# Kernel optimization log

Hardware: AMD Instinct MI355X
Metric: run time of the kernel (lower is better)

## Reference

```python
import jax, jax.numpy as jnp
import numpy as np

B, D_IN, UNITS = 16384, 4096, 4096
EPS = 1e-05

def setup_inputs() -> dict:
    key = jax.random.key(0)
    k1, k2 = jax.random.split(key)
    x = jax.random.normal(k1, (B, D_IN), dtype=jnp.float32)
    # glorot_uniform init for Dense kernel
    limit = np.sqrt(6.0 / (D_IN + UNITS)).astype(np.float32)
    W = jax.random.uniform(k2, (D_IN, UNITS), dtype=jnp.float32, minval=-limit, maxval=limit)
    b = jnp.zeros((UNITS,), dtype=jnp.float32)
    return {"x": x, "W": W, "b": b}

def reference(x, W, b):
    # L2-normalize each row (tf.norm axis=1, keepdims) with +1e-5 stabilizer
    x_norm = jnp.sqrt(jnp.sum(x * x, axis=1, keepdims=True)) + EPS  # [B,1]
    x_dir = x / x_norm                                              # [B,D]
    # dense + bias + ReLU
    return jax.nn.relu(x_dir @ W + b)                               # [B,UNITS]
```

## Files before the change

### kernel.cpp

```cpp
#include <hip/hip_runtime.h>

#define BROWS 16384
#define DIN   4096
#define NOUT  4096
#define EPSV  1e-5f

typedef __attribute__((ext_vector_type(8))) short short8;
typedef __attribute__((ext_vector_type(4))) float f32x4;

__device__ __forceinline__ unsigned short f32_to_bf16(float f) {
    union { float f; unsigned u; } v;
    v.f = f;
    unsigned r = (v.u + 0x7fffu + ((v.u >> 16) & 1u)) >> 16;
    return (unsigned short)r;
}

__global__ __launch_bounds__(256) void normalize_cast_kernel(
    const float* __restrict__ x, unsigned short* __restrict__ A) {
    const int row = blockIdx.x;
    const int tid = threadIdx.x;
    const float4* xr = (const float4*)(x + (size_t)row * DIN);
    float4 v[4];
    float ss = 0.f;
#pragma unroll
    for (int i = 0; i < 4; ++i) {
        v[i] = xr[tid + i * 256];
        ss += v[i].x * v[i].x + v[i].y * v[i].y + v[i].z * v[i].z + v[i].w * v[i].w;
    }
#pragma unroll
    for (int o = 32; o > 0; o >>= 1) ss += __shfl_down(ss, o);
    __shared__ float red[4];
    const int wave = tid >> 6, lane = tid & 63;
    if (lane == 0) red[wave] = ss;
    __syncthreads();
    const float inv = 1.f / (sqrtf(red[0] + red[1] + red[2] + red[3]) + EPSV);
    uint2* Ar = (uint2*)(A + (size_t)row * DIN);
#pragma unroll
    for (int i = 0; i < 4; ++i) {
        uint2 p;
        p.x = (unsigned)f32_to_bf16(v[i].x * inv) | ((unsigned)f32_to_bf16(v[i].y * inv) << 16);
        p.y = (unsigned)f32_to_bf16(v[i].z * inv) | ((unsigned)f32_to_bf16(v[i].w * inv) << 16);
        Ar[tid + i * 256] = p;
    }
}

__global__ __launch_bounds__(256) void transpose_cast_kernel(
    const float* __restrict__ W, unsigned short* __restrict__ Wt) {
    __shared__ float tile[32][33];
    const int bn = blockIdx.x * 32, bk = blockIdx.y * 32;
    const int t = threadIdx.x;
    const int lk = t >> 3, ln4 = (t & 7) * 4;
    float4 v = *(const float4*)(W + (size_t)(bk + lk) * NOUT + bn + ln4);
    tile[lk][ln4 + 0] = v.x;
    tile[lk][ln4 + 1] = v.y;
    tile[lk][ln4 + 2] = v.z;
    tile[lk][ln4 + 3] = v.w;
    __syncthreads();
    const int ln = t >> 3, lk4 = (t & 7) * 4;
    uint2 p;
    p.x = (unsigned)f32_to_bf16(tile[lk4 + 0][ln]) | ((unsigned)f32_to_bf16(tile[lk4 + 1][ln]) << 16);
    p.y = (unsigned)f32_to_bf16(tile[lk4 + 2][ln]) | ((unsigned)f32_to_bf16(tile[lk4 + 3][ln]) << 16);
    *(uint2*)(Wt + (size_t)(bn + ln) * DIN + bk + lk4) = p;
}


__device__ __forceinline__ void async_copy16(const unsigned short* g, unsigned short* l) {
    __builtin_amdgcn_global_load_lds(
        (const __attribute__((address_space(1))) unsigned int*)g,
        (__attribute__((address_space(3))) unsigned int*)l, 16, 0, 0);
}

__global__ __launch_bounds__(256, 2) void gemm_bias_relu_kernel(
    const unsigned short* __restrict__ A, const unsigned short* __restrict__ Wt,
    const float* __restrict__ bias, float* __restrict__ C) {
    __shared__ __align__(16) unsigned short As[128 * 32];
    __shared__ __align__(16) unsigned short Bs[128 * 32];
    const int tid = threadIdx.x;
    const int wave = tid >> 6, lane = tid & 63;
    const int m0 = blockIdx.y * 128, n0 = blockIdx.x * 128;
    const int wr = (wave >> 1) * 64, wc = (wave & 1) * 64;
    const int lm = lane & 15;
    const int lk8 = (lane >> 4) * 8;

    f32x4 acc[4][4] = {};

    const int c0 = tid, c1 = tid + 256;
    const unsigned short* gA0 = A + (size_t)(m0 + (c0 >> 2)) * DIN + (c0 & 3) * 8;
    const unsigned short* gA1 = A + (size_t)(m0 + (c1 >> 2)) * DIN + (c1 & 3) * 8;
    const unsigned short* gB0 = Wt + (size_t)(n0 + (c0 >> 2)) * DIN + (c0 & 3) * 8;
    const unsigned short* gB1 = Wt + (size_t)(n0 + (c1 >> 2)) * DIN + (c1 & 3) * 8;
    unsigned short* lA0 = &As[(c0 & ~63) * 8];
    unsigned short* lA1 = &As[(c1 & ~63) * 8];
    unsigned short* lB0 = &Bs[(c0 & ~63) * 8];
    unsigned short* lB1 = &Bs[(c1 & ~63) * 8];

    for (int k0 = 0; k0 < DIN; k0 += 32) {
        __syncthreads();
        async_copy16(gA0 + k0, lA0);
        async_copy16(gA1 + k0, lA1);
        async_copy16(gB0 + k0, lB0);
        async_copy16(gB1 + k0, lB1);
        __syncthreads();

        short8 af[4], bf[4];
#pragma unroll
        for (int i = 0; i < 4; ++i)
            af[i] = *(const short8*)(&As[(wr + i * 16 + lm) * 32 + lk8]);
#pragma unroll
        for (int j = 0; j < 4; ++j)
            bf[j] = *(const short8*)(&Bs[(wc + j * 16 + lm) * 32 + lk8]);
#pragma unroll
        for (int i = 0; i < 4; ++i)
#pragma unroll
            for (int j = 0; j < 4; ++j)
                acc[i][j] = __builtin_amdgcn_mfma_f32_16x16x32_bf16(af[i], bf[j], acc[i][j], 0, 0, 0);
    }

    float bj[4];
#pragma unroll
    for (int j = 0; j < 4; ++j) bj[j] = bias[n0 + wc + j * 16 + lm];
    const int colb = n0 + wc + lm;
    const int rowb = m0 + wr + ((lane >> 4) << 2);
#pragma unroll
    for (int i = 0; i < 4; ++i) {
#pragma unroll
        for (int r = 0; r < 4; ++r) {
            float* cp = C + (size_t)(rowb + i * 16 + r) * NOUT + colb;
#pragma unroll
            for (int j = 0; j < 4; ++j) {
                float v = acc[i][j][r] + bj[j];
                cp[j * 16] = v > 0.f ? v : 0.f;
            }
        }
    }
}

extern "C" void kernel_launch(void* const* d_in, const int* in_sizes, int n_in,
                              void* d_out, int out_size, void* d_ws, size_t ws_size,
                              hipStream_t stream) {
    const float* x = (const float*)d_in[0];
    const float* W = (const float*)d_in[1];
    const float* b = (const float*)d_in[2];
    float* out = (float*)d_out;

    unsigned short* Abf = (unsigned short*)d_ws;
    unsigned short* Wt = Abf + (size_t)BROWS * DIN;

    normalize_cast_kernel<<<BROWS, 256, 0, stream>>>(x, Abf);
    transpose_cast_kernel<<<dim3(NOUT / 32, DIN / 32), 256, 0, stream>>>(W, Wt);
    gemm_bias_relu_kernel<<<dim3(NOUT / 128, BROWS / 128), 256, 0, stream>>>(Abf, Wt, b, out);
}
```

Before: 1.082 ms.

## Swizzle GEMM LDS layout, use nontemporal output stores, enlarge transpose tiles

The GEMM now XOR-swizzles the k-chunk position in LDS per row, both when filling it through global_load_lds and when reading MFMA fragments, to reduce LDS bank conflicts on the short8 reads. Output stores become nontemporal so the large fp32 result bypasses cache retention. The W transpose/cast kernel moves to 64x64 tiles with four loads per thread to amortise launch and sync overhead. The swizzle must stay consistent between the global source offsets and the fragment reads, or results will be wrong.

After: 1.070 ms. Within noise of the previous version (-1.1%).

```diff
diff --git a/kernel.cpp b/kernel.cpp
--- a/kernel.cpp
+++ b/kernel.cpp
@@ -46,21 +46,28 @@
 
 __global__ __launch_bounds__(256) void transpose_cast_kernel(
     const float* __restrict__ W, unsigned short* __restrict__ Wt) {
-    __shared__ float tile[32][33];
-    const int bn = blockIdx.x * 32, bk = blockIdx.y * 32;
+    __shared__ float tile[64][65];
+    const int bn = blockIdx.x * 64, bk = blockIdx.y * 64;
     const int t = threadIdx.x;
-    const int lk = t >> 3, ln4 = (t & 7) * 4;
-    float4 v = *(const float4*)(W + (size_t)(bk + lk) * NOUT + bn + ln4);
-    tile[lk][ln4 + 0] = v.x;
-    tile[lk][ln4 + 1] = v.y;
-    tile[lk][ln4 + 2] = v.z;
-    tile[lk][ln4 + 3] = v.w;
+    const int lk = t >> 4, ln4 = (t & 15) * 4;
+#pragma unroll
+    for (int i = 0; i < 4; ++i) {
+        float4 v = *(const float4*)(W + (size_t)(bk + lk + i * 16) * NOUT + bn + ln4);
+        tile[lk + i * 16][ln4 + 0] = v.x;
+        tile[lk + i * 16][ln4 + 1] = v.y;
+        tile[lk + i * 16][ln4 + 2] = v.z;
+        tile[lk + i * 16][ln4 + 3] = v.w;
+    }
     __syncthreads();
-    const int ln = t >> 3, lk4 = (t & 7) * 4;
-    uint2 p;
-    p.x = (unsigned)f32_to_bf16(tile[lk4 + 0][ln]) | ((unsigned)f32_to_bf16(tile[lk4 + 1][ln]) << 16);
-    p.y = (unsigned)f32_to_bf16(tile[lk4 + 2][ln]) | ((unsigned)f32_to_bf16(tile[lk4 + 3][ln]) << 16);
-    *(uint2*)(Wt + (size_t)(bn + ln) * DIN + bk + lk4) = p;
+    const int ln = t >> 4, lk4 = (t & 15) * 4;
+#pragma unroll
+    for (int i = 0; i < 4; ++i) {
+        const int n = ln + i * 16;
+        uint2 p;
+        p.x = (unsigned)f32_to_bf16(tile[lk4 + 0][n]) | ((unsigned)f32_to_bf16(tile[lk4 + 1][n]) << 16);
+        p.y = (unsigned)f32_to_bf16(tile[lk4 + 2][n]) | ((unsigned)f32_to_bf16(tile[lk4 + 3][n]) << 16);
+        *(uint2*)(Wt + (size_t)(bn + n) * DIN + bk + lk4) = p;
+    }
 }
 
 
@@ -80,15 +87,19 @@
     const int m0 = blockIdx.y * 128, n0 = blockIdx.x * 128;
     const int wr = (wave >> 1) * 64, wc = (wave & 1) * 64;
     const int lm = lane & 15;
-    const int lk8 = (lane >> 4) * 8;
+    const int q = lane >> 4;
+    const int sw = (lm >> 1) & 3;
+    const int ksl = (q ^ sw) * 8;
 
     f32x4 acc[4][4] = {};
 
     const int c0 = tid, c1 = tid + 256;
-    const unsigned short* gA0 = A + (size_t)(m0 + (c0 >> 2)) * DIN + (c0 & 3) * 8;
-    const unsigned short* gA1 = A + (size_t)(m0 + (c1 >> 2)) * DIN + (c1 & 3) * 8;
-    const unsigned short* gB0 = Wt + (size_t)(n0 + (c0 >> 2)) * DIN + (c0 & 3) * 8;
-    const unsigned short* gB1 = Wt + (size_t)(n0 + (c1 >> 2)) * DIN + (c1 & 3) * 8;
+    const int p0 = ((c0 & 3) ^ ((c0 >> 3) & 3)) * 8;
+    const int p1 = ((c1 & 3) ^ ((c1 >> 3) & 3)) * 8;
+    const unsigned short* gA0 = A + (size_t)(m0 + (c0 >> 2)) * DIN + p0;
+    const unsigned short* gA1 = A + (size_t)(m0 + (c1 >> 2)) * DIN + p1;
+    const unsigned short* gB0 = Wt + (size_t)(n0 + (c0 >> 2)) * DIN + p0;
+    const unsigned short* gB1 = Wt + (size_t)(n0 + (c1 >> 2)) * DIN + p1;
     unsigned short* lA0 = &As[(c0 & ~63) * 8];
     unsigned short* lA1 = &As[(c1 & ~63) * 8];
     unsigned short* lB0 = &Bs[(c0 & ~63) * 8];
@@ -105,10 +116,10 @@
         short8 af[4], bf[4];
 #pragma unroll
         for (int i = 0; i < 4; ++i)
-            af[i] = *(const short8*)(&As[(wr + i * 16 + lm) * 32 + lk8]);
+            af[i] = *(const short8*)(&As[(wr + i * 16 + lm) * 32 + ksl]);
 #pragma unroll
         for (int j = 0; j < 4; ++j)
-            bf[j] = *(const short8*)(&Bs[(wc + j * 16 + lm) * 32 + lk8]);
+            bf[j] = *(const short8*)(&Bs[(wc + j * 16 + lm) * 32 + ksl]);
 #pragma unroll
         for (int i = 0; i < 4; ++i)
 #pragma unroll
@@ -120,7 +131,7 @@
 #pragma unroll
     for (int j = 0; j < 4; ++j) bj[j] = bias[n0 + wc + j * 16 + lm];
     const int colb = n0 + wc + lm;
-    const int rowb = m0 + wr + ((lane >> 4) << 2);
+    const int rowb = m0 + wr + (q << 2);
 #pragma unroll
     for (int i = 0; i < 4; ++i) {
 #pragma unroll
@@ -129,7 +140,7 @@
 #pragma unroll
             for (int j = 0; j < 4; ++j) {
                 float v = acc[i][j][r] + bj[j];
-                cp[j * 16] = v > 0.f ? v : 0.f;
+                __builtin_nontemporal_store(v > 0.f ? v : 0.f, cp + j * 16);
             }
         }
     }
@@ -147,6 +158,6 @@
     unsigned short* Wt = Abf + (size_t)BROWS * DIN;
 
     normalize_cast_kernel<<<BROWS, 256, 0, stream>>>(x, Abf);
-    transpose_cast_kernel<<<dim3(NOUT / 32, DIN / 32), 256, 0, stream>>>(W, Wt);
+    transpose_cast_kernel<<<dim3(NOUT / 64, DIN / 64), 256, 0, stream>>>(W, Wt);
     gemm_bias_relu_kernel<<<dim3(NOUT / 128, BROWS / 128), 256, 0, stream>>>(Abf, Wt, b, out);
 }
```
